# Kernel tuning notes

Hardware: AMD Instinct MI355X
Metric: run time of the kernel (lower is better)

## Reference

```python
import jax, jax.numpy as jnp
import numpy as np

N_NODES = 100000
N_EDGES = 1600000
D = 64
N_LAYERS = 5
N_GRAPHS = 256


def setup_inputs() -> dict:
    key = jax.random.key(0)
    ks = jax.random.split(key, 12)
    x = jax.random.normal(ks[0], (N_NODES, D), dtype=jnp.float32)
    edge_index = jax.random.randint(ks[1], (2, N_EDGES), 0, N_NODES, dtype=jnp.int64)
    batch = jnp.sort(jax.random.randint(ks[2], (N_NODES,), 0, N_GRAPHS, dtype=jnp.int64))
    s = 1.0 / np.sqrt(D)
    # stacked GINConv MLP params: Linear(D,D) -> ReLU -> Linear(D,D), per layer
    Ws1 = jax.random.uniform(ks[3], (N_LAYERS, D, D), jnp.float32, -s, s)
    bs1 = jax.random.uniform(ks[4], (N_LAYERS, D), jnp.float32, -s, s)
    Ws2 = jax.random.uniform(ks[5], (N_LAYERS, D, D), jnp.float32, -s, s)
    bs2 = jax.random.uniform(ks[6], (N_LAYERS, D), jnp.float32, -s, s)
    # final readout MLP: Linear(D,D) -> ReLU -> Linear(D,D)
    mW1 = jax.random.uniform(ks[7], (D, D), jnp.float32, -s, s)
    mb1 = jax.random.uniform(ks[8], (D,), jnp.float32, -s, s)
    mW2 = jax.random.uniform(ks[9], (D, D), jnp.float32, -s, s)
    mb2 = jax.random.uniform(ks[10], (D,), jnp.float32, -s, s)
    return {"x": x, "edge_index": edge_index, "batch": batch,
            "Ws1": Ws1, "bs1": bs1, "Ws2": Ws2, "bs2": bs2,
            "mW1": mW1, "mb1": mb1, "mW2": mW2, "mb2": mb2}


def reference(x, edge_index, batch, Ws1, bs1, Ws2, bs2, mW1, mb1, mW2, mb2):
    src, dst = edge_index[0], edge_index[1]
    h = x
    for l in range(N_LAYERS):
        # GINConv (eps=0): MLP(h + sum_{j in N(i)} h_j)
        agg = jax.ops.segment_sum(h[src], dst, num_segments=N_NODES)
        z = h + agg
        z = jax.nn.relu(z @ Ws1[l] + bs1[l])
        h = z @ Ws2[l] + bs2[l]
    # global mean pool over graphs
    sums = jax.ops.segment_sum(h, batch, num_segments=N_GRAPHS)
    cnts = jax.ops.segment_sum(jnp.ones((h.shape[0],), h.dtype), batch, num_segments=N_GRAPHS)
    pooled = sums / jnp.maximum(cnts, 1.0)[:, None]
    # readout MLP
    out = jax.nn.relu(pooled @ mW1 + mb1) @ mW2 + mb2
    return out
```

## Files before the change

### kernel.cpp

```cpp
#include <hip/hip_runtime.h>
#include <hip/hip_bf16.h>

#define N_NODES 100000
#define N_EDGES 1600000
#define DIM 64
#define N_LAYERS 5
#define N_GRAPHS 256

#define NB2 196
#define SUBCAP2 9216
#define CAP2 12800
#define DUMMY N_NODES
#define TILE 3200
#define NTILE 500
#define MTILES (N_NODES / 16)

typedef __attribute__((ext_vector_type(8))) short short8;
typedef __attribute__((ext_vector_type(4))) float float4v;

__global__ void zero_kernel(int* p, int n) {
    int i = blockIdx.x * blockDim.x + threadIdx.x;
    if (i < n) p[i] = 0;
}

__device__ __forceinline__ unsigned short f2bf(float f) {
    unsigned int u = __float_as_uint(f);
    unsigned int r = (u + 0x7fffu + ((u >> 16) & 1u)) >> 16;
    return (unsigned short)r;
}
__device__ __forceinline__ float bf2f(unsigned short b) {
    return __uint_as_float(((unsigned int)b) << 16);
}

__global__ void zero_dummy_kernel(unsigned short* a, unsigned short* b) {
    int t = threadIdx.x;
    a[(size_t)DUMMY * DIM + t] = 0;
    b[(size_t)DUMMY * DIM + t] = 0;
}

__global__ void cvt_kernel(const float4* __restrict__ x, ushort4* __restrict__ hb, int n4) {
    int i = blockIdx.x * blockDim.x + threadIdx.x;
    if (i < n4) {
        float4 v = x[i];
        ushort4 o;
        o.x = f2bf(v.x); o.y = f2bf(v.y); o.z = f2bf(v.z); o.w = f2bf(v.w);
        hb[i] = o;
    }
}

__global__ void prepack_kernel(const float* __restrict__ Ws1, const float* __restrict__ Ws2,
                               unsigned short* __restrict__ wpk) {
    int t = blockIdx.x * blockDim.x + threadIdx.x;
    if (t >= N_LAYERS * 32 * 64) return;
    int lane = t & 63;
    int frag = (t >> 6) & 31;
    int l = t >> 11;
    int kf = frag & 1;
    int nt = (frag >> 1) & 3;
    int split = (frag >> 3) & 1;
    int mat = (frag >> 4) & 1;
    const float* W = (mat ? Ws2 : Ws1) + (size_t)l * DIM * DIM;
    unsigned short outv[8];
#pragma unroll
    for (int j = 0; j < 8; ++j) {
        int k = kf * 32 + ((lane >> 4) << 3) + j;
        int n = nt * 16 + (lane & 15);
        float v = W[k * DIM + n];
        unsigned short hi = f2bf(v);
        outv[j] = split ? f2bf(v - bf2f(hi)) : hi;
    }
    ushort4* dst = (ushort4*)(wpk + ((size_t)(l * 32 + frag) * 64 + lane) * 8);
    dst[0] = make_ushort4(outv[0], outv[1], outv[2], outv[3]);
    dst[1] = make_ushort4(outv[4], outv[5], outv[6], outv[7]);
}

__global__ __launch_bounds__(256) void bin_kernel(
    const int* __restrict__ src, const int* __restrict__ dst,
    int* __restrict__ bcursor, int* __restrict__ pairbuf) {
    __shared__ int hcnt[NB2];
    __shared__ int gbase[NB2];
    __shared__ int lcur[NB2];
    const int tid = threadIdx.x;
    const int base = blockIdx.x * TILE;

    for (int l = tid; l < NB2; l += 256) { hcnt[l] = 0; lcur[l] = 0; }
    __syncthreads();
    for (int j = tid; j < TILE; j += 256) {
        int d = dst[base + j];
        atomicAdd(&hcnt[d >> 9], 1);
    }
    __syncthreads();
    for (int l = tid; l < NB2; l += 256)
        gbase[l] = atomicAdd(&bcursor[l], hcnt[l]);
    __syncthreads();
    for (int j = tid; j < TILE; j += 256) {
        int s = src[base + j];
        int d = dst[base + j];
        int b = d >> 9;
        int r = atomicAdd(&lcur[b], 1);
        int pos = gbase[b] + r;
        if (pos < SUBCAP2) pairbuf[b * SUBCAP2 + pos] = (s << 9) | (d & 511);
    }
}

__global__ __launch_bounds__(256) void csr_kernel(
    const int* __restrict__ bcursor, const int* __restrict__ pairbuf,
    int* __restrict__ esrc, int2* __restrict__ meta) {
    __shared__ int lcnt[512];
    __shared__ int loff[512];
    __shared__ int lcur[512];
    __shared__ int s2[256];
    const int b = blockIdx.x;
    const int tid = threadIdx.x;
    int ec = bcursor[b];
    if (ec > SUBCAP2) ec = SUBCAP2;
    const int* pp = pairbuf + b * SUBCAP2;

    for (int l = tid; l < 512; l += 256) lcnt[l] = 0;
    __syncthreads();
    for (int j = tid; j < ec; j += 256) atomicAdd(&lcnt[pp[j] & 511], 1);
    __syncthreads();

    int c0 = (lcnt[2 * tid] + 7) & ~7;
    int c1 = (lcnt[2 * tid + 1] + 7) & ~7;
    s2[tid] = c0 + c1;
    __syncthreads();
    for (int off = 1; off < 256; off <<= 1) {
        int v = (tid >= off) ? s2[tid - off] : 0;
        __syncthreads();
        s2[tid] += v;
        __syncthreads();
    }
    int exc = s2[tid] - (c0 + c1);
    loff[2 * tid] = exc;
    loff[2 * tid + 1] = exc + c0;
    __syncthreads();

    int* eb = esrc + (size_t)b * CAP2;
    for (int l = tid; l < 512; l += 256) {
        int st = loff[l];
        int cn = lcnt[l];
        int cp = (cn + 7) & ~7;
        lcur[l] = st;
        int node = b * 512 + l;
        if (node < N_NODES) meta[node] = make_int2(b * CAP2 + st, cp);
        for (int j = cn; j < cp; ++j) eb[st + j] = DUMMY;
    }
    __syncthreads();

    for (int j = tid; j < ec; j += 256) {
        int p = pp[j];
        int pos = atomicAdd(&lcur[p & 511], 1);
        eb[pos] = p >> 9;
    }
}

__device__ __forceinline__ void acc8(float* acc, uint4 v) {
    acc[0] += __uint_as_float(v.x << 16);
    acc[1] += __uint_as_float(v.x & 0xffff0000u);
    acc[2] += __uint_as_float(v.y << 16);
    acc[3] += __uint_as_float(v.y & 0xffff0000u);
    acc[4] += __uint_as_float(v.z << 16);
    acc[5] += __uint_as_float(v.z & 0xffff0000u);
    acc[6] += __uint_as_float(v.w << 16);
    acc[7] += __uint_as_float(v.w & 0xffff0000u);
}

__global__ __launch_bounds__(256) void agg_kernel(
    const unsigned short* __restrict__ hin, unsigned short* __restrict__ z,
    const int2* __restrict__ meta, const int* __restrict__ esrc, int n_nodes) {
    __shared__ float zbuf[4][2][8][DIM];
    const int lane = threadIdx.x & 63;
    const int wv = threadIdx.x >> 6;
    const int grp = lane >> 3;
    const int sub = lane & 7;
    const int wave_id = (blockIdx.x * blockDim.x + threadIdx.x) >> 6;
    const int n_waves = (gridDim.x * blockDim.x) >> 6;
    const uint4* __restrict__ h4 = (const uint4*)hin;

    for (int ii = wave_id; 2 * ii < n_nodes; ii += n_waves) {
        const int iA = 2 * ii;
        const int iB = iA + 1;
        const int2 mA = meta[iA];
        const int2 mB = meta[iB];
        const float selfA = bf2f(hin[iA * DIM + lane]);
        const float selfB = bf2f(hin[iB * DIM + lane]);
        const int* eA = esrc + mA.x + grp;
        const int* eB = esrc + mB.x + grp;
        const int nA = mA.y, nB = mB.y;

        float accA[8], accB[8];
#pragma unroll
        for (int j = 0; j < 8; ++j) { accA[j] = 0.f; accB[j] = 0.f; }

        int k = 0;
        const int nmin = (nA < nB) ? nA : nB;
        for (; k < nmin; k += 8) {
            const int ia = eA[k];
            const int ib = eB[k];
            uint4 va = h4[ia * 8 + sub];
            uint4 vb = h4[ib * 8 + sub];
            acc8(accA, va);
            acc8(accB, vb);
        }
        for (int kk = k; kk < nA; kk += 8) {
            uint4 va = h4[eA[kk] * 8 + sub];
            acc8(accA, va);
        }
        for (int kk = k; kk < nB; kk += 8) {
            uint4 vb = h4[eB[kk] * 8 + sub];
            acc8(accB, vb);
        }

        *((float4*)&zbuf[wv][0][grp][sub * 8 + 0]) = make_float4(accA[0], accA[1], accA[2], accA[3]);
        *((float4*)&zbuf[wv][0][grp][sub * 8 + 4]) = make_float4(accA[4], accA[5], accA[6], accA[7]);
        *((float4*)&zbuf[wv][1][grp][sub * 8 + 0]) = make_float4(accB[0], accB[1], accB[2], accB[3]);
        *((float4*)&zbuf[wv][1][grp][sub * 8 + 4]) = make_float4(accB[4], accB[5], accB[6], accB[7]);
        __builtin_amdgcn_wave_barrier();
        float zA = selfA, zB = selfB;
#pragma unroll
        for (int g = 0; g < 8; ++g) {
            zA += zbuf[wv][0][g][lane];
            zB += zbuf[wv][1][g][lane];
        }
        z[iA * DIM + lane] = f2bf(zA);
        z[iB * DIM + lane] = f2bf(zB);
        __builtin_amdgcn_wave_barrier();
    }
}

__device__ __forceinline__ short8 load_frag(const unsigned short* __restrict__ wl, int frag, int lane) {
    union { uint4 u; short8 s; } c;
    c.u = *(const uint4*)(wl + ((size_t)(frag * 64 + lane)) * 8);
    return c.s;
}

__device__ __forceinline__ void split8(const float* v, short8& hi, short8& lo) {
#pragma unroll
    for (int j = 0; j < 8; ++j) {
        unsigned short h = f2bf(v[j]);
        hi[j] = (short)h;
        lo[j] = (short)f2bf(v[j] - bf2f(h));
    }
}

__global__ __launch_bounds__(256) void mlp_mfma_kernel(
    const unsigned short* __restrict__ z, unsigned short* __restrict__ hout,
    const unsigned short* __restrict__ wl,
    const float* __restrict__ b1, const float* __restrict__ b2) {
    __shared__ float tbuf[4][16][68];
    const int lane = threadIdx.x & 63;
    const int wv = threadIdx.x >> 6;
    const int m = lane & 15;
    const int quad = lane >> 4;
    const int wave_id = (blockIdx.x * blockDim.x + threadIdx.x) >> 6;
    const int n_waves = (gridDim.x * blockDim.x) >> 6;

    float b1v[4], b2v[4];
#pragma unroll
    for (int nt = 0; nt < 4; ++nt) {
        b1v[nt] = b1[nt * 16 + m];
        b2v[nt] = b2[nt * 16 + m];
    }

    for (int tile = wave_id; tile < MTILES; tile += n_waves) {
        const int node0 = tile * 16;

        short8 a1[2];
#pragma unroll
        for (int kf = 0; kf < 2; ++kf) {
            union { uint4 u; short8 s; } c;
            c.u = *(const uint4*)(z + ((size_t)(node0 + m)) * DIM + kf * 32 + quad * 8);
            a1[kf] = c.s;
        }

        float4v acc1[4] = {};
#pragma unroll
        for (int nt = 0; nt < 4; ++nt) {
#pragma unroll
            for (int kf = 0; kf < 2; ++kf) {
                short8 bhi = load_frag(wl, ((0 * 2 + 0) * 4 + nt) * 2 + kf, lane);
                short8 blo = load_frag(wl, ((0 * 2 + 1) * 4 + nt) * 2 + kf, lane);
                acc1[nt] = __builtin_amdgcn_mfma_f32_16x16x32_bf16(a1[kf], bhi, acc1[nt], 0, 0, 0);
                acc1[nt] = __builtin_amdgcn_mfma_f32_16x16x32_bf16(a1[kf], blo, acc1[nt], 0, 0, 0);
            }
        }

#pragma unroll
        for (int nt = 0; nt < 4; ++nt) {
#pragma unroll
            for (int r = 0; r < 4; ++r) {
                float tv = acc1[nt][r] + b1v[nt];
                tbuf[wv][quad * 4 + r][nt * 16 + m] = fmaxf(tv, 0.f);
            }
        }
        __builtin_amdgcn_wave_barrier();

        short8 a2hi[2], a2lo[2];
#pragma unroll
        for (int kf = 0; kf < 2; ++kf) {
            const float4* tp = (const float4*)&tbuf[wv][m][kf * 32 + quad * 8];
            float4 t0 = tp[0];
            float4 t1 = tp[1];
            float v[8] = {t0.x, t0.y, t0.z, t0.w, t1.x, t1.y, t1.z, t1.w};
            split8(v, a2hi[kf], a2lo[kf]);
        }
        __builtin_amdgcn_wave_barrier();

        float4v acc2[4] = {};
#pragma unroll
        for (int nt = 0; nt < 4; ++nt) {
#pragma unroll
            for (int kf = 0; kf < 2; ++kf) {
                short8 bhi = load_frag(wl, ((1 * 2 + 0) * 4 + nt) * 2 + kf, lane);
                short8 blo = load_frag(wl, ((1 * 2 + 1) * 4 + nt) * 2 + kf, lane);
                acc2[nt] = __builtin_amdgcn_mfma_f32_16x16x32_bf16(a2hi[kf], bhi, acc2[nt], 0, 0, 0);
                acc2[nt] = __builtin_amdgcn_mfma_f32_16x16x32_bf16(a2hi[kf], blo, acc2[nt], 0, 0, 0);
                acc2[nt] = __builtin_amdgcn_mfma_f32_16x16x32_bf16(a2lo[kf], bhi, acc2[nt], 0, 0, 0);
            }
        }

#pragma unroll
        for (int nt = 0; nt < 4; ++nt) {
#pragma unroll
            for (int r = 0; r < 4; ++r) {
                float o = acc2[nt][r] + b2v[nt];
                hout[((size_t)(node0 + quad * 4 + r)) * DIM + nt * 16 + m] = f2bf(o);
            }
        }
    }
}

__global__ __launch_bounds__(256) void pool_mlp_kernel(
    const unsigned short* __restrict__ h, const int* __restrict__ batch,
    const float* __restrict__ mW1, const float* __restrict__ mb1,
    const float* __restrict__ mW2, const float* __restrict__ mb2,
    float* __restrict__ out, int n_nodes) {
    __shared__ float part[4][DIM];
    const int g = blockIdx.x;
    const int lane = threadIdx.x & 63;
    const int w = threadIdx.x >> 6;

    int lo = 0, hi = n_nodes;
    while (lo < hi) {
        int mid = (lo + hi) >> 1;
        if (batch[mid] < g) lo = mid + 1; else hi = mid;
    }
    const int s0 = lo;
    hi = n_nodes;
    while (lo < hi) {
        int mid = (lo + hi) >> 1;
        if (batch[mid] < g + 1) lo = mid + 1; else hi = mid;
    }
    const int e0 = lo;

    float acc = 0.f;
    int i = s0 + w;
    for (; i + 12 < e0; i += 16) {
        float v0 = bf2f(h[i * DIM + lane]);
        float v1 = bf2f(h[(i + 4) * DIM + lane]);
        float v2 = bf2f(h[(i + 8) * DIM + lane]);
        float v3 = bf2f(h[(i + 12) * DIM + lane]);
        acc += (v0 + v1) + (v2 + v3);
    }
    for (; i < e0; i += 4) acc += bf2f(h[i * DIM + lane]);
    part[w][lane] = acc;
    __syncthreads();

    if (w == 0) {
        acc = (part[0][lane] + part[1][lane]) + (part[2][lane] + part[3][lane]);
        float cntf = (float)(e0 - s0);
        acc /= fmaxf(cntf, 1.f);

        float t = mb1[lane];
#pragma unroll
        for (int d = 0; d < DIM; ++d) {
            float zd = __shfl(acc, d);
            t = fmaf(zd, mW1[d * DIM + lane], t);
        }
        t = fmaxf(t, 0.f);
        float o = mb2[lane];
#pragma unroll
        for (int d = 0; d < DIM; ++d) {
            float rd = __shfl(t, d);
            o = fmaf(rd, mW2[d * DIM + lane], o);
        }
        out[g * DIM + lane] = o;
    }
}

extern "C" void kernel_launch(void* const* d_in, const int* in_sizes, int n_in,
                              void* d_out, int out_size, void* d_ws, size_t ws_size,
                              hipStream_t stream) {
    const float* x   = (const float*)d_in[0];
    const int*   ei  = (const int*)d_in[1];
    const int*   bat = (const int*)d_in[2];
    const float* Ws1 = (const float*)d_in[3];
    const float* bs1 = (const float*)d_in[4];
    const float* Ws2 = (const float*)d_in[5];
    const float* bs2 = (const float*)d_in[6];
    const float* mW1 = (const float*)d_in[7];
    const float* mb1 = (const float*)d_in[8];
    const float* mW2 = (const float*)d_in[9];
    const float* mb2 = (const float*)d_in[10];
    float* out = (float*)d_out;

    char* ws = (char*)d_ws;
    size_t off = 0;
    auto alloc = [&](size_t bytes) {
        void* p = ws + off;
        off += (bytes + 255) & ~(size_t)255;
        return p;
    };
    int*  esrc    = (int*)alloc((size_t)NB2 * CAP2 * 4);
    int2* meta    = (int2*)alloc((size_t)N_NODES * 8);
    unsigned short* hbfA = (unsigned short*)alloc(((size_t)N_NODES + 1) * DIM * 2);
    unsigned short* hbfB = (unsigned short*)alloc(((size_t)N_NODES + 1) * DIM * 2);
    int*  bcursor = (int*)alloc((size_t)NB2 * 4);
    unsigned short* wpk = (unsigned short*)alloc((size_t)N_LAYERS * 32 * 64 * 8 * 2);
    void* uni = alloc((size_t)NB2 * SUBCAP2 * 4);
    int*   pairbuf = (int*)uni;
    unsigned short* zb = (unsigned short*)uni;
    (void)zb;
    unsigned short* zbig = (unsigned short*)alloc((size_t)N_NODES * DIM * 2);

    const int* src = ei;
    const int* dst = ei + N_EDGES;

    zero_kernel<<<1, 256, 0, stream>>>(bcursor, NB2);
    bin_kernel<<<NTILE, 256, 0, stream>>>(src, dst, bcursor, pairbuf);
    csr_kernel<<<NB2, 256, 0, stream>>>(bcursor, pairbuf, esrc, meta);

    prepack_kernel<<<(N_LAYERS * 32 * 64 + 255) / 256, 256, 0, stream>>>(Ws1, Ws2, wpk);
    zero_dummy_kernel<<<1, 64, 0, stream>>>(hbfA, hbfB);
    cvt_kernel<<<(N_NODES * DIM / 4 + 255) / 256, 256, 0, stream>>>(
        (const float4*)x, (ushort4*)hbfA, N_NODES * DIM / 4);

    const unsigned short* hin = hbfA;
    unsigned short* hout = hbfB;
    for (int l = 0; l < N_LAYERS; ++l) {
        agg_kernel<<<2048, 256, 0, stream>>>(hin, zbig, meta, esrc, N_NODES);
        mlp_mfma_kernel<<<1024, 256, 0, stream>>>(zbig, hout,
                                                  wpk + (size_t)l * 32 * 64 * 8,
                                                  bs1 + (size_t)l * DIM,
                                                  bs2 + (size_t)l * DIM);
        hin = hout;
        hout = (hout == hbfA) ? hbfB : hbfA;
    }
    pool_mlp_kernel<<<N_GRAPHS, 256, 0, stream>>>(hin, bat, mW1, mb1, mW2, mb2, out, N_NODES);
}
```

Baseline: 371.9 us.

## Merge init kernels, split pooling across blocks with atomics, resize MLP grid

Folds the zeroing, weight-prepack, dummy-row clear and fp32-to-bf16 conversion into one init kernel, cutting several tiny launches. The mean-pool is split into a 4-blocks-per-graph atomic sum kernel plus a small readout kernel, which raises parallelism in the pooling phase. The MLP kernel grid grows from 1024 to 1563 blocks. The atomics make the summation order nondeterministic, and the pairbuf buffer no longer shares space with an alias, which uses a little more workspace.

```diff
diff --git a/kernel.cpp b/kernel.cpp
--- a/kernel.cpp
+++ b/kernel.cpp
@@ -18,11 +18,6 @@
 typedef __attribute__((ext_vector_type(8))) short short8;
 typedef __attribute__((ext_vector_type(4))) float float4v;
 
-__global__ void zero_kernel(int* p, int n) {
-    int i = blockIdx.x * blockDim.x + threadIdx.x;
-    if (i < n) p[i] = 0;
-}
-
 __device__ __forceinline__ unsigned short f2bf(float f) {
     unsigned int u = __float_as_uint(f);
     unsigned int r = (u + 0x7fffu + ((u >> 16) & 1u)) >> 16;
@@ -32,13 +27,12 @@
     return __uint_as_float(((unsigned int)b) << 16);
 }
 
-__global__ void zero_dummy_kernel(unsigned short* a, unsigned short* b) {
-    int t = threadIdx.x;
-    a[(size_t)DUMMY * DIM + t] = 0;
-    b[(size_t)DUMMY * DIM + t] = 0;
-}
-
-__global__ void cvt_kernel(const float4* __restrict__ x, ushort4* __restrict__ hb, int n4) {
+__global__ __launch_bounds__(256) void cvt_init_kernel(
+    const float4* __restrict__ x, ushort4* __restrict__ hb,
+    const float* __restrict__ Ws1, const float* __restrict__ Ws2,
+    unsigned short* __restrict__ wpk,
+    unsigned short* __restrict__ hbfA, unsigned short* __restrict__ hbfB,
+    int* __restrict__ bcursor, float* __restrict__ pooled, int n4) {
     int i = blockIdx.x * blockDim.x + threadIdx.x;
     if (i < n4) {
         float4 v = x[i];
@@ -46,32 +40,34 @@
         o.x = f2bf(v.x); o.y = f2bf(v.y); o.z = f2bf(v.z); o.w = f2bf(v.w);
         hb[i] = o;
     }
-}
-
-__global__ void prepack_kernel(const float* __restrict__ Ws1, const float* __restrict__ Ws2,
-                               unsigned short* __restrict__ wpk) {
-    int t = blockIdx.x * blockDim.x + threadIdx.x;
-    if (t >= N_LAYERS * 32 * 64) return;
-    int lane = t & 63;
-    int frag = (t >> 6) & 31;
-    int l = t >> 11;
-    int kf = frag & 1;
-    int nt = (frag >> 1) & 3;
-    int split = (frag >> 3) & 1;
-    int mat = (frag >> 4) & 1;
-    const float* W = (mat ? Ws2 : Ws1) + (size_t)l * DIM * DIM;
-    unsigned short outv[8];
-#pragma unroll
-    for (int j = 0; j < 8; ++j) {
-        int k = kf * 32 + ((lane >> 4) << 3) + j;
-        int n = nt * 16 + (lane & 15);
-        float v = W[k * DIM + n];
-        unsigned short hi = f2bf(v);
-        outv[j] = split ? f2bf(v - bf2f(hi)) : hi;
-    }
-    ushort4* dst = (ushort4*)(wpk + ((size_t)(l * 32 + frag) * 64 + lane) * 8);
-    dst[0] = make_ushort4(outv[0], outv[1], outv[2], outv[3]);
-    dst[1] = make_ushort4(outv[4], outv[5], outv[6], outv[7]);
+    if (i < N_LAYERS * 32 * 64) {
+        int lane = i & 63;
+        int frag = (i >> 6) & 31;
+        int l = i >> 11;
+        int kf = frag & 1;
+        int nt = (frag >> 1) & 3;
+        int split = (frag >> 3) & 1;
+        int mat = (frag >> 4) & 1;
+        const float* W = (mat ? Ws2 : Ws1) + (size_t)l * DIM * DIM;
+        unsigned short outv[8];
+#pragma unroll
+        for (int j = 0; j < 8; ++j) {
+            int k = kf * 32 + ((lane >> 4) << 3) + j;
+            int n = nt * 16 + (lane & 15);
+            float v = W[k * DIM + n];
+            unsigned short hi = f2bf(v);
+            outv[j] = split ? f2bf(v - bf2f(hi)) : hi;
+        }
+        ushort4* dst = (ushort4*)(wpk + ((size_t)(l * 32 + frag) * 64 + lane) * 8);
+        dst[0] = make_ushort4(outv[0], outv[1], outv[2], outv[3]);
+        dst[1] = make_ushort4(outv[4], outv[5], outv[6], outv[7]);
+    }
+    if (i < N_GRAPHS * DIM) pooled[i] = 0.f;
+    if (i < NB2) bcursor[i] = 0;
+    if (i < DIM) {
+        hbfA[(size_t)DUMMY * DIM + i] = 0;
+        hbfB[(size_t)DUMMY * DIM + i] = 0;
+    }
 }
 
 __global__ __launch_bounds__(256) void bin_kernel(
@@ -331,13 +327,11 @@
     }
 }
 
-__global__ __launch_bounds__(256) void pool_mlp_kernel(
+__global__ __launch_bounds__(256) void pool_sum_kernel(
     const unsigned short* __restrict__ h, const int* __restrict__ batch,
-    const float* __restrict__ mW1, const float* __restrict__ mb1,
-    const float* __restrict__ mW2, const float* __restrict__ mb2,
-    float* __restrict__ out, int n_nodes) {
-    __shared__ float part[4][DIM];
-    const int g = blockIdx.x;
+    float* __restrict__ pooled, int n_nodes) {
+    const int g = blockIdx.x >> 2;
+    const int p = blockIdx.x & 3;
     const int lane = threadIdx.x & 63;
     const int w = threadIdx.x >> 6;
 
@@ -355,38 +349,48 @@
     const int e0 = lo;
 
     float acc = 0.f;
-    int i = s0 + w;
-    for (; i + 12 < e0; i += 16) {
-        float v0 = bf2f(h[i * DIM + lane]);
-        float v1 = bf2f(h[(i + 4) * DIM + lane]);
-        float v2 = bf2f(h[(i + 8) * DIM + lane]);
-        float v3 = bf2f(h[(i + 12) * DIM + lane]);
-        acc += (v0 + v1) + (v2 + v3);
-    }
-    for (; i < e0; i += 4) acc += bf2f(h[i * DIM + lane]);
-    part[w][lane] = acc;
-    __syncthreads();
-
-    if (w == 0) {
-        acc = (part[0][lane] + part[1][lane]) + (part[2][lane] + part[3][lane]);
-        float cntf = (float)(e0 - s0);
-        acc /= fmaxf(cntf, 1.f);
-
-        float t = mb1[lane];
-#pragma unroll
-        for (int d = 0; d < DIM; ++d) {
-            float zd = __shfl(acc, d);
-            t = fmaf(zd, mW1[d * DIM + lane], t);
-        }
-        t = fmaxf(t, 0.f);
-        float o = mb2[lane];
-#pragma unroll
-        for (int d = 0; d < DIM; ++d) {
-            float rd = __shfl(t, d);
-            o = fmaf(rd, mW2[d * DIM + lane], o);
-        }
-        out[g * DIM + lane] = o;
-    }
+    for (int i = s0 + p * 4 + w; i < e0; i += 16)
+        acc += bf2f(h[(size_t)i * DIM + lane]);
+    atomicAdd(&pooled[g * DIM + lane], acc);
+}
+
+__global__ __launch_bounds__(64) void pool_read_kernel(
+    const float* __restrict__ pooled, const int* __restrict__ batch,
+    const float* __restrict__ mW1, const float* __restrict__ mb1,
+    const float* __restrict__ mW2, const float* __restrict__ mb2,
+    float* __restrict__ out, int n_nodes) {
+    const int g = blockIdx.x;
+    const int lane = threadIdx.x;
+
+    int lo = 0, hi = n_nodes;
+    while (lo < hi) {
+        int mid = (lo + hi) >> 1;
+        if (batch[mid] < g) lo = mid + 1; else hi = mid;
+    }
+    const int s0 = lo;
+    hi = n_nodes;
+    while (lo < hi) {
+        int mid = (lo + hi) >> 1;
+        if (batch[mid] < g + 1) lo = mid + 1; else hi = mid;
+    }
+    const int e0 = lo;
+
+    float acc = pooled[g * DIM + lane] / fmaxf((float)(e0 - s0), 1.f);
+
+    float t = mb1[lane];
+#pragma unroll
+    for (int d = 0; d < DIM; ++d) {
+        float zd = __shfl(acc, d);
+        t = fmaf(zd, mW1[d * DIM + lane], t);
+    }
+    t = fmaxf(t, 0.f);
+    float o = mb2[lane];
+#pragma unroll
+    for (int d = 0; d < DIM; ++d) {
+        float rd = __shfl(t, d);
+        o = fmaf(rd, mW2[d * DIM + lane], o);
+    }
+    out[g * DIM + lane] = o;
 }
 
 extern "C" void kernel_launch(void* const* d_in, const int* in_sizes, int n_in,
@@ -418,34 +422,31 @@
     unsigned short* hbfB = (unsigned short*)alloc(((size_t)N_NODES + 1) * DIM * 2);
     int*  bcursor = (int*)alloc((size_t)NB2 * 4);
     unsigned short* wpk = (unsigned short*)alloc((size_t)N_LAYERS * 32 * 64 * 8 * 2);
-    void* uni = alloc((size_t)NB2 * SUBCAP2 * 4);
-    int*   pairbuf = (int*)uni;
-    unsigned short* zb = (unsigned short*)uni;
-    (void)zb;
+    float* pooled = (float*)alloc((size_t)N_GRAPHS * DIM * 4);
+    int*   pairbuf = (int*)alloc((size_t)NB2 * SUBCAP2 * 4);
     unsigned short* zbig = (unsigned short*)alloc((size_t)N_NODES * DIM * 2);
 
     const int* src = ei;
     const int* dst = ei + N_EDGES;
 
-    zero_kernel<<<1, 256, 0, stream>>>(bcursor, NB2);
+    cvt_init_kernel<<<(N_NODES * DIM / 4 + 255) / 256, 256, 0, stream>>>(
+        (const float4*)x, (ushort4*)hbfA, Ws1, Ws2, wpk, hbfA, hbfB,
+        bcursor, pooled, N_NODES * DIM / 4);
+
     bin_kernel<<<NTILE, 256, 0, stream>>>(src, dst, bcursor, pairbuf);
     csr_kernel<<<NB2, 256, 0, stream>>>(bcursor, pairbuf, esrc, meta);
-
-    prepack_kernel<<<(N_LAYERS * 32 * 64 + 255) / 256, 256, 0, stream>>>(Ws1, Ws2, wpk);
-    zero_dummy_kernel<<<1, 64, 0, stream>>>(hbfA, hbfB);
-    cvt_kernel<<<(N_NODES * DIM / 4 + 255) / 256, 256, 0, stream>>>(
-        (const float4*)x, (ushort4*)hbfA, N_NODES * DIM / 4);
 
     const unsigned short* hin = hbfA;
     unsigned short* hout = hbfB;
     for (int l = 0; l < N_LAYERS; ++l) {
         agg_kernel<<<2048, 256, 0, stream>>>(hin, zbig, meta, esrc, N_NODES);
-        mlp_mfma_kernel<<<1024, 256, 0, stream>>>(zbig, hout,
+        mlp_mfma_kernel<<<1563, 256, 0, stream>>>(zbig, hout,
                                                   wpk + (size_t)l * 32 * 64 * 8,
                                                   bs1 + (size_t)l * DIM,
                                                   bs2 + (size_t)l * DIM);
         hin = hout;
         hout = (hout == hbfA) ? hbfB : hbfA;
     }
-    pool_mlp_kernel<<<N_GRAPHS, 256, 0, stream>>>(hin, bat, mW1, mb1, mW2, mb2, out, N_NODES);
-}
+    pool_sum_kernel<<<N_GRAPHS * 4, 256, 0, stream>>>(hin, bat, pooled, N_NODES);
+    pool_read_kernel<<<N_GRAPHS, 64, 0, stream>>>(pooled, bat, mW1, mb1, mW2, mb2, out, N_NODES);
+}
```

Result: slower. 387.9 us (+4.3%).
